# Kernel tuning notes

Measured on AMD Instinct MI355X. Metric: run time of the kernel, lower is better.

The kernel has to match this reference:

```python
import jax, jax.numpy as jnp
import numpy as np

F = 32          # number of fields
B = 2048        # batch size
K = 64          # embedding dim
H = 64          # attention hidden size
VOCAB = 100000  # hash_size


def setup_inputs() -> dict:
    key = jax.random.key(0)
    ks = jax.random.split(key, 7)
    x = jax.random.randint(ks[0], (F, B), 0, VOCAB)
    emb_v = jax.random.normal(ks[1], (VOCAB, K), jnp.float32) * 0.05
    at_w = jax.random.normal(ks[2], (K, H), jnp.float32) * 0.1
    at_b = jnp.zeros((H,), jnp.float32)
    at_h = jax.random.normal(ks[3], (H, 1), jnp.float32) * 0.1
    p = jax.random.normal(ks[4], (K, 1), jnp.float32) * 0.1
    w0 = jnp.zeros((), jnp.float32)
    w1 = jax.random.normal(ks[5], (VOCAB, 1), jnp.float32) * 0.05
    return {"x": x, "emb_v": emb_v, "at_w": at_w, "at_b": at_b,
            "at_h": at_h, "p": p, "w0": w0, "w1": w1}


def reference(x, emb_v, at_w, at_b, at_h, p, w0, w1):
    # Embedding lookup: [F, B, K]
    V = emb_v[x]
    # Pairwise interactions: all i<j pairs -> [P, B, K], P = F*(F-1)/2
    iu, ju = np.triu_indices(F, k=1)
    VV = V[iu] * V[ju]                                   # [P, B, K]
    # Attention MLP per pair (no softmax in original code)
    hid = jax.nn.relu(jnp.einsum('pbk,kh->pbh', VV, at_w) + at_b)  # [P, B, H]
    score = jnp.einsum('pbh,ho->pbo', hid, at_h)         # [P, B, 1]
    # Attention-weighted sum pooling over pairs -> [B, K]
    pooled = jnp.sum(VV * score, axis=0)
    # Second-order score
    at_fm_score = pooled @ p                             # [B, 1]
    # First-order FM part: sum over fields of w1 lookups
    fm1 = w0 + jnp.sum(w1[x], axis=0)                    # [B, 1]
    logit = at_fm_score + fm1
    prob = jax.nn.sigmoid(logit)
    return prob
```

## Files before the change

### kernel.cpp

```cpp
#include <hip/hip_runtime.h>
#include <math.h>

#define F      32
#define BATCH  2048
#define K      64
#define H      64
#define NPAIR  496
#define NTROW  31

#define WS_BFRAG_SHORTS (5 * 2 * 64 * 8)
#define WS_PAIRS_OFF    10240

typedef float v4f __attribute__((ext_vector_type(4)));
typedef short v8s __attribute__((ext_vector_type(8)));

__device__ __forceinline__ float bf2f(short s) {
    union { unsigned u; float f; } v;
    v.u = ((unsigned)(unsigned short)s) << 16;
    return v.f;
}
__device__ __forceinline__ short f2bf(float f) {
    union { float f; unsigned u; } v; v.f = f;
    unsigned r = v.u + 0x7fffu + ((v.u >> 16) & 1u);
    return (short)(r >> 16);
}

__global__ void afm_setup(const float* __restrict__ at_w,
                          const float* __restrict__ p,
                          short* __restrict__ bfrag_ws,
                          int*   __restrict__ pairs_ws)
{
    int idx = blockIdx.x * blockDim.x + threadIdx.x;

    if (idx < 5 * 2 * 64) {
        int nt   = idx >> 7;
        int rem  = idx & 127;
        int kk   = rem >> 6;
        int lane = rem & 63;
        int quad = lane >> 4, c = lane & 15;
        v8s w;
        #pragma unroll
        for (int e = 0; e < 8; ++e) {
            int k = kk * 32 + quad * 8 + e;
            float val = (nt < 4) ? at_w[k * H + nt * 16 + c] : p[k];
            w[e] = f2bf(val);
        }
        *(v8s*)&bfrag_ws[idx * 8] = w;
    }

    if (idx < NTROW * 16) {
        int tr = idx >> 4, c = idx & 15;
        int pr = tr * 16 + c;
        int i = 0, rem = pr;
        while (rem >= F - 1 - i) { rem -= F - 1 - i; ++i; }
        int j = i + 1 + rem;
        int packed = i | (j << 8);
        #pragma unroll
        for (int q = 0; q < 4; ++q)
            pairs_ws[tr * 64 + q * 16 + c] = packed;
    }
}

__global__ __launch_bounds__(256)
void afm_fwd(const int*   __restrict__ x,
             const float* __restrict__ emb_v,
             const float* __restrict__ at_b,
             const float* __restrict__ at_h,
             const float* __restrict__ w0,
             const float* __restrict__ w1,
             const short* __restrict__ bfrag_ws,
             const int*   __restrict__ pairs_ws,
             float*       __restrict__ out)
{
    __shared__ __align__(16) short Vsh[F][72];
    __shared__ float fm_sh[F];
    __shared__ float wacc[4];

    const int b    = blockIdx.x;
    const int t    = threadIdx.x;
    const int lane = t & 63;
    const int wv   = t >> 6;
    const int c    = lane & 15;
    const int quad = lane >> 4;

    {
        int f  = t >> 3;
        int cb = (t & 7) * 8;
        int idx = x[f * BATCH + b];
        const float4* src = (const float4*)&emb_v[idx * K + cb];
        float4 a0 = src[0], a1 = src[1];
        v8s w;
        w[0] = f2bf(a0.x); w[1] = f2bf(a0.y); w[2] = f2bf(a0.z); w[3] = f2bf(a0.w);
        w[4] = f2bf(a1.x); w[5] = f2bf(a1.y); w[6] = f2bf(a1.z); w[7] = f2bf(a1.w);
        *(v8s*)&Vsh[f][cb] = w;
    }
    if (t < F) fm_sh[t] = w1[x[t * BATCH + b]];

    v8s bf[5][2];
    #pragma unroll
    for (int nt = 0; nt < 5; ++nt)
        #pragma unroll
        for (int kk = 0; kk < 2; ++kk)
            bf[nt][kk] = *(const v8s*)&bfrag_ws[((nt * 2 + kk) * 64 + lane) * 8];

    float ab[4], ah[4];
    #pragma unroll
    for (int nt = 0; nt < 4; ++nt) {
        ab[nt] = at_b[nt * 16 + c];
        ah[nt] = at_h[nt * 16 + c];
    }

    int prk[8];
    #pragma unroll
    for (int s = 0; s < 8; ++s) {
        int tr = wv + 4 * s;
        prk[s] = (tr < NTROW) ? pairs_ws[tr * 64 + lane] : 0;
    }

    __syncthreads();

    float accTot = 0.f;

    #pragma unroll
    for (int s = 0; s < 8; ++s) {
        int tr = wv + 4 * s;
        if (tr >= NTROW) break;
        int pi = prk[s] & 255, pj = (prk[s] >> 8) & 255;

        v8s af[2];
        #pragma unroll
        for (int kk = 0; kk < 2; ++kk) {
            v8s vi = *(const v8s*)&Vsh[pi][kk * 32 + quad * 8];
            v8s vj = *(const v8s*)&Vsh[pj][kk * 32 + quad * 8];
            #pragma unroll
            for (int e = 0; e < 8; ++e)
                af[kk][e] = f2bf(bf2f(vi[e]) * bf2f(vj[e]));
        }

        v4f acc[5];
        #pragma unroll
        for (int nt = 0; nt < 5; ++nt) {
            acc[nt] = (v4f){0.f, 0.f, 0.f, 0.f};
            #pragma unroll
            for (int kk = 0; kk < 2; ++kk)
                acc[nt] = __builtin_amdgcn_mfma_f32_16x16x32_bf16(af[kk], bf[nt][kk], acc[nt], 0, 0, 0);
        }

        #pragma unroll
        for (int r = 0; r < 4; ++r) {
            float sp = 0.f;
            #pragma unroll
            for (int nt = 0; nt < 4; ++nt)
                sp = fmaf(fmaxf(acc[nt][r] + ab[nt], 0.f), ah[nt], sp);
            accTot = fmaf(acc[4][r], sp, accTot);
        }
    }

    accTot += __shfl_xor(accTot, 1);
    accTot += __shfl_xor(accTot, 2);
    accTot += __shfl_xor(accTot, 4);
    accTot += __shfl_xor(accTot, 8);
    accTot += __shfl_xor(accTot, 16);
    accTot += __shfl_xor(accTot, 32);
    if (lane == 0) wacc[wv] = accTot;
    __syncthreads();

    if (t == 0) {
        float fm1 = w0[0];
        #pragma unroll
        for (int f = 0; f < F; ++f) fm1 += fm_sh[f];
        float logit = wacc[0] + wacc[1] + wacc[2] + wacc[3] + fm1;
        out[b] = 1.f / (1.f + expf(-logit));
    }
}

extern "C" void kernel_launch(void* const* d_in, const int* in_sizes, int n_in,
                              void* d_out, int out_size, void* d_ws, size_t ws_size,
                              hipStream_t stream) {
    const int*   x     = (const int*)  d_in[0];
    const float* emb_v = (const float*)d_in[1];
    const float* at_w  = (const float*)d_in[2];
    const float* at_b  = (const float*)d_in[3];
    const float* at_h  = (const float*)d_in[4];
    const float* p     = (const float*)d_in[5];
    const float* w0    = (const float*)d_in[6];
    const float* w1    = (const float*)d_in[7];
    float* out = (float*)d_out;

    short* bfrag_ws = (short*)d_ws;
    int*   pairs_ws = (int*)((char*)d_ws + WS_PAIRS_OFF);

    afm_setup<<<3, 256, 0, stream>>>(at_w, p, bfrag_ws, pairs_ws);
    afm_fwd<<<BATCH, 256, 0, stream>>>(x, emb_v, at_b, at_h, w0, w1,
                                       bfrag_ws, pairs_ws, out);
}
```

Measured before the change: 108.1 us.

## Switch MFMA path to fp16 with packed products and software-prefetched pair loads

Replaces the bf16 data path with fp16, so the elementwise pair products become packed half multiplies instead of per-element bf16 unpack/multiply/repack, and the MFMA becomes the f16 variant. The bias is folded into the accumulator init, and the shared-memory loads for the next pair tile are issued before the current MFMAs to overlap LDS latency. The loop is made branch-free by always running 8 iterations and guarding only the reduction, which adds wasted MFMA work on one wave. fp16 has less range than bf16, though the embedding values here are small.

```diff
diff --git a/kernel.cpp b/kernel.cpp
--- a/kernel.cpp
+++ b/kernel.cpp
@@ -8,27 +8,15 @@
 #define NPAIR  496
 #define NTROW  31
 
-#define WS_BFRAG_SHORTS (5 * 2 * 64 * 8)
 #define WS_PAIRS_OFF    10240
 
-typedef float v4f __attribute__((ext_vector_type(4)));
-typedef short v8s __attribute__((ext_vector_type(8)));
-
-__device__ __forceinline__ float bf2f(short s) {
-    union { unsigned u; float f; } v;
-    v.u = ((unsigned)(unsigned short)s) << 16;
-    return v.f;
-}
-__device__ __forceinline__ short f2bf(float f) {
-    union { float f; unsigned u; } v; v.f = f;
-    unsigned r = v.u + 0x7fffu + ((v.u >> 16) & 1u);
-    return (short)(r >> 16);
-}
+typedef float    v4f __attribute__((ext_vector_type(4)));
+typedef _Float16 v8h __attribute__((ext_vector_type(8)));
 
 __global__ void afm_setup(const float* __restrict__ at_w,
                           const float* __restrict__ p,
-                          short* __restrict__ bfrag_ws,
-                          int*   __restrict__ pairs_ws)
+                          _Float16* __restrict__ bfrag_ws,
+                          int*      __restrict__ pairs_ws)
 {
     int idx = blockIdx.x * blockDim.x + threadIdx.x;
 
@@ -38,14 +26,14 @@
         int kk   = rem >> 6;
         int lane = rem & 63;
         int quad = lane >> 4, c = lane & 15;
-        v8s w;
+        v8h w;
         #pragma unroll
         for (int e = 0; e < 8; ++e) {
             int k = kk * 32 + quad * 8 + e;
             float val = (nt < 4) ? at_w[k * H + nt * 16 + c] : p[k];
-            w[e] = f2bf(val);
+            w[e] = (_Float16)val;
         }
-        *(v8s*)&bfrag_ws[idx * 8] = w;
+        *(v8h*)&bfrag_ws[idx * 8] = w;
     }
 
     if (idx < NTROW * 16) {
@@ -68,11 +56,11 @@
              const float* __restrict__ at_h,
              const float* __restrict__ w0,
              const float* __restrict__ w1,
-             const short* __restrict__ bfrag_ws,
+             const _Float16* __restrict__ bfrag_ws,
              const int*   __restrict__ pairs_ws,
              float*       __restrict__ out)
 {
-    __shared__ __align__(16) short Vsh[F][72];
+    __shared__ __align__(16) _Float16 Vsh[F][72];
     __shared__ float fm_sh[F];
     __shared__ float wacc[4];
 
@@ -89,19 +77,21 @@
         int idx = x[f * BATCH + b];
         const float4* src = (const float4*)&emb_v[idx * K + cb];
         float4 a0 = src[0], a1 = src[1];
-        v8s w;
-        w[0] = f2bf(a0.x); w[1] = f2bf(a0.y); w[2] = f2bf(a0.z); w[3] = f2bf(a0.w);
-        w[4] = f2bf(a1.x); w[5] = f2bf(a1.y); w[6] = f2bf(a1.z); w[7] = f2bf(a1.w);
-        *(v8s*)&Vsh[f][cb] = w;
+        v8h w;
+        w[0] = (_Float16)a0.x; w[1] = (_Float16)a0.y;
+        w[2] = (_Float16)a0.z; w[3] = (_Float16)a0.w;
+        w[4] = (_Float16)a1.x; w[5] = (_Float16)a1.y;
+        w[6] = (_Float16)a1.z; w[7] = (_Float16)a1.w;
+        *(v8h*)&Vsh[f][cb] = w;
     }
     if (t < F) fm_sh[t] = w1[x[t * BATCH + b]];
 
-    v8s bf[5][2];
+    v8h bf[5][2];
     #pragma unroll
     for (int nt = 0; nt < 5; ++nt)
         #pragma unroll
         for (int kk = 0; kk < 2; ++kk)
-            bf[nt][kk] = *(const v8s*)&bfrag_ws[((nt * 2 + kk) * 64 + lane) * 8];
+            bf[nt][kk] = *(const v8h*)&bfrag_ws[((nt * 2 + kk) * 64 + lane) * 8];
 
     float ab[4], ah[4];
     #pragma unroll
@@ -121,38 +111,44 @@
 
     float accTot = 0.f;
 
+    v8h vi0 = *(const v8h*)&Vsh[prk[0] & 255][quad * 8];
+    v8h vj0 = *(const v8h*)&Vsh[(prk[0] >> 8) & 255][quad * 8];
+    v8h vi1 = *(const v8h*)&Vsh[prk[0] & 255][32 + quad * 8];
+    v8h vj1 = *(const v8h*)&Vsh[(prk[0] >> 8) & 255][32 + quad * 8];
+
     #pragma unroll
     for (int s = 0; s < 8; ++s) {
-        int tr = wv + 4 * s;
-        if (tr >= NTROW) break;
-        int pi = prk[s] & 255, pj = (prk[s] >> 8) & 255;
+        v8h af0 = vi0 * vj0;
+        v8h af1 = vi1 * vj1;
 
-        v8s af[2];
-        #pragma unroll
-        for (int kk = 0; kk < 2; ++kk) {
-            v8s vi = *(const v8s*)&Vsh[pi][kk * 32 + quad * 8];
-            v8s vj = *(const v8s*)&Vsh[pj][kk * 32 + quad * 8];
-            #pragma unroll
-            for (int e = 0; e < 8; ++e)
-                af[kk][e] = f2bf(bf2f(vi[e]) * bf2f(vj[e]));
+        if (s < 7) {
+            int pi = prk[s + 1] & 255, pj = (prk[s + 1] >> 8) & 255;
+            vi0 = *(const v8h*)&Vsh[pi][quad * 8];
+            vj0 = *(const v8h*)&Vsh[pj][quad * 8];
+            vi1 = *(const v8h*)&Vsh[pi][32 + quad * 8];
+            vj1 = *(const v8h*)&Vsh[pj][32 + quad * 8];
         }
 
         v4f acc[5];
         #pragma unroll
+        for (int nt = 0; nt < 4; ++nt)
+            acc[nt] = (v4f){ab[nt], ab[nt], ab[nt], ab[nt]};
+        acc[4] = (v4f){0.f, 0.f, 0.f, 0.f};
+        #pragma unroll
         for (int nt = 0; nt < 5; ++nt) {
-            acc[nt] = (v4f){0.f, 0.f, 0.f, 0.f};
-            #pragma unroll
-            for (int kk = 0; kk < 2; ++kk)
-                acc[nt] = __builtin_amdgcn_mfma_f32_16x16x32_bf16(af[kk], bf[nt][kk], acc[nt], 0, 0, 0);
+            acc[nt] = __builtin_amdgcn_mfma_f32_16x16x32_f16(af0, bf[nt][0], acc[nt], 0, 0, 0);
+            acc[nt] = __builtin_amdgcn_mfma_f32_16x16x32_f16(af1, bf[nt][1], acc[nt], 0, 0, 0);
         }
 
-        #pragma unroll
-        for (int r = 0; r < 4; ++r) {
-            float sp = 0.f;
+        if (wv + 4 * s < NTROW) {
             #pragma unroll
-            for (int nt = 0; nt < 4; ++nt)
-                sp = fmaf(fmaxf(acc[nt][r] + ab[nt], 0.f), ah[nt], sp);
-            accTot = fmaf(acc[4][r], sp, accTot);
+            for (int r = 0; r < 4; ++r) {
+                float sp = 0.f;
+                #pragma unroll
+                for (int nt = 0; nt < 4; ++nt)
+                    sp = fmaf(fmaxf(acc[nt][r], 0.f), ah[nt], sp);
+                accTot = fmaf(acc[4][r], sp, accTot);
+            }
         }
     }
 
@@ -187,8 +183,8 @@
     const float* w1    = (const float*)d_in[7];
     float* out = (float*)d_out;
 
-    short* bfrag_ws = (short*)d_ws;
-    int*   pairs_ws = (int*)((char*)d_ws + WS_PAIRS_OFF);
+    _Float16* bfrag_ws = (_Float16*)d_ws;
+    int*      pairs_ws = (int*)((char*)d_ws + WS_PAIRS_OFF);
 
     afm_setup<<<3, 256, 0, stream>>>(at_w, p, bfrag_ws, pairs_ws);
     afm_fwd<<<BATCH, 256, 0, stream>>>(x, emb_v, at_b, at_h, w0, w1,
```

Measured after the change: 99.63 us. 7.8% less time.
